# Kernel tuning notes

Hardware: AMD Instinct MI355X
Metric: run time of the kernel (lower is better)

## Reference

```python
import jax, jax.numpy as jnp
import numpy as np

EPS = 1e-6
ROPE_BASE = 10000.0

def setup_inputs() -> dict:
    key = jax.random.key(0)
    ks = jax.random.split(key, 6)
    B, S, D = 4, 4096, 1024
    NS, DS = 4, D // 4          # num_subspaces, subspace_dim
    H = 2 * DS                  # hidden_dim = ff_multiplier * subspace_dim
    scale = 0.02
    return {
        "x": jax.random.normal(ks[0], (B, S, D), dtype=jnp.float32),
        "norm_w": jnp.ones((D,), dtype=jnp.float32),
        # grouped SwiGLU weights: [NS, in, out] layout so we can einsum directly
        "Wg": jax.random.normal(ks[1], (NS, DS, H), dtype=jnp.float32) * scale,
        "Wu": jax.random.normal(ks[2], (NS, DS, H), dtype=jnp.float32) * scale,
        "Wd": jax.random.normal(ks[3], (NS, H, DS), dtype=jnp.float32) * scale,
        "Wo": jax.random.normal(ks[4], (D, D), dtype=jnp.float32) * scale,
    }

def _rope_cos_sin(S, D, dtype):
    inv_freq = 1.0 / (ROPE_BASE ** (jnp.arange(0, D, 2, dtype=jnp.float32) / D))
    freqs = jnp.arange(S, dtype=jnp.float32)[:, None] * inv_freq[None, :]  # [S, D/2]
    emb = jnp.concatenate([freqs, freqs], axis=-1)                          # [S, D]
    return jnp.cos(emb).astype(dtype), jnp.sin(emb).astype(dtype)

def reference(x, norm_w, Wg, Wu, Wd, Wo):
    B, S, D = x.shape
    NS, DS, H = Wg.shape
    # RMSNorm
    h = x * jax.lax.rsqrt(jnp.mean(x * x, axis=-1, keepdims=True) + EPS) * norm_w
    # RoPE over full hidden dim (rotate_half convention)
    cos, sin = _rope_cos_sin(S, D, x.dtype)
    half = D // 2
    rot = jnp.concatenate([-h[..., half:], h[..., :half]], axis=-1)
    h = h * cos[None] + rot * sin[None]
    # Grouped SwiGLU over NS independent subspaces
    hc = h.reshape(B, S, NS, DS)
    gate = jax.nn.silu(jnp.einsum('bsnd,ndh->bsnh', hc, Wg))
    up = jnp.einsum('bsnd,ndh->bsnh', hc, Wu)
    down = jnp.einsum('bsnh,nhd->bsnd', gate * up, Wd)
    out = down.reshape(B, S, D)
    # Final projection + residual
    return jnp.einsum('bsd,de->bse', out, Wo) + x
```

## Files before the change

### kernel.cpp

```cpp
#include <hip/hip_runtime.h>

typedef unsigned short u16;
typedef unsigned int   u32;

typedef float  f32x4  __attribute__((ext_vector_type(4)));
typedef __bf16 bf16x8 __attribute__((ext_vector_type(8)));

#define S_LEN  4096
#define DMODEL 1024
#define NSUB   4
#define DSUB   256
#define HFF    512
#define NTOK   16384

static_assert(sizeof(bf16x8) == 16, "frag size");

__device__ __forceinline__ u16 f2bf(float f) {
    union { float f; u32 u; } v; v.f = f;
    u32 r = (v.u + 0x7fffu + ((v.u >> 16) & 1u)) >> 16;
    return (u16)r;
}

#define MFMA16(a, b, c) __builtin_amdgcn_mfma_f32_16x16x32_bf16((a), (b), (c), 0, 0, 0)

__device__ __forceinline__ void gl_lds16(const void* g, void* l) {
    __builtin_amdgcn_global_load_lds(
        (const __attribute__((address_space(1))) void*)g,
        (__attribute__((address_space(3))) void*)l,
        16, 0, 0);
}
#define LGKM0 asm volatile("s_waitcnt lgkmcnt(0)" ::: "memory")
#define SCHED0 __builtin_amdgcn_sched_barrier(0)
#define SBAR __builtin_amdgcn_s_barrier()

__global__ __launch_bounds__(256) void k_prep(const float* __restrict__ Wg,
                                              const float* __restrict__ Wu,
                                              const float* __restrict__ Wd,
                                              const float* __restrict__ Wo,
                                              const float* __restrict__ x,
                                              const float* __restrict__ nw,
                                              u16* __restrict__ wgP,
                                              u16* __restrict__ wuP,
                                              u16* __restrict__ wdP,
                                              u16* __restrict__ woP,
                                              u16* __restrict__ h) {
    int bid = blockIdx.x;
    int tid = threadIdx.x;
    if (bid < 1280) {
        __shared__ float tl[32][65];
        const float* src; u16* dst; int K, C, rel;
        if (bid < 256)      { src = Wg; dst = wgP; K = 256;  C = 512;  rel = bid; }
        else if (bid < 512) { src = Wu; dst = wuP; K = 256;  C = 512;  rel = bid - 256; }
        else if (bid < 768) { src = Wd; dst = wdP; K = 512;  C = 256;  rel = bid - 512; }
        else                { src = Wo; dst = woP; K = 1024; C = 1024; rel = bid - 768; }
        int ncb = C >> 6, nkt = K >> 5;
        int cb = rel % ncb; int r2 = rel / ncb;
        int kt = r2 % nkt;  int b  = r2 / nkt;
        {
            int r = tid >> 3, c0 = (tid & 7) * 8;
            const float* s = src + ((size_t)(b * K + kt * 32 + r)) * C + cb * 64 + c0;
            float4 v0 = *(const float4*)(s);
            float4 v1 = *(const float4*)(s + 4);
            tl[r][c0 + 0] = v0.x; tl[r][c0 + 1] = v0.y; tl[r][c0 + 2] = v0.z; tl[r][c0 + 3] = v0.w;
            tl[r][c0 + 4] = v1.x; tl[r][c0 + 5] = v1.y; tl[r][c0 + 6] = v1.z; tl[r][c0 + 7] = v1.w;
        }
        __syncthreads();
        {
            int f = tid >> 6, l = tid & 63;
            union { u16 v[8]; uint4 q; } u;
#pragma unroll
            for (int j = 0; j < 8; ++j)
                u.v[j] = f2bf(tl[(l >> 4) * 8 + j][f * 16 + (l & 15)]);
            size_t ctile = (size_t)(b * (C >> 4) + cb * 4 + f);
            *(uint4*)(dst + (ctile * nkt + kt) * 512 + l * 8) = u.q;
        }
        return;
    }
    int tok = bid - 1280;
    int s = tok & (S_LEN - 1);
    int t = tid;
    const float* xr = x + (size_t)tok * DMODEL;
    float x0 = xr[t], x1 = xr[t + 256], x2 = xr[t + 512], x3 = xr[t + 768];
    float ss = x0 * x0 + x1 * x1 + x2 * x2 + x3 * x3;
#pragma unroll
    for (int o = 32; o > 0; o >>= 1) ss += __shfl_down(ss, o, 64);
    __shared__ float red[4];
    if ((t & 63) == 0) red[t >> 6] = ss;
    __syncthreads();
    float tot = red[0] + red[1] + red[2] + red[3];
    float sc = rsqrtf(tot * (1.0f / DMODEL) + 1e-6f);
    float n0 = x0 * sc * nw[t];
    float n1 = x1 * sc * nw[t + 256];
    float n2 = x2 * sc * nw[t + 512];
    float n3 = x3 * sc * nw[t + 768];
    const float C = -0.017988946039015984f;
    float sf = (float)s;
    float ang0 = sf * expf(C * (float)t);
    float ang1 = sf * expf(C * (float)(t + 256));
    float sn0, cs0, sn1, cs1;
    sincosf(ang0, &sn0, &cs0);
    sincosf(ang1, &sn1, &cs1);
    u16* hr = h + (size_t)tok * DMODEL;
    hr[t]       = f2bf(n0 * cs0 - n2 * sn0);
    hr[t + 256] = f2bf(n1 * cs1 - n3 * sn1);
    hr[t + 512] = f2bf(n2 * cs0 + n0 * sn0);
    hr[t + 768] = f2bf(n3 * cs1 + n1 * sn1);
}

__global__ __launch_bounds__(512, 2)
void k_swiglu(const u16* __restrict__ h,
              const u16* __restrict__ wgP,
              const u16* __restrict__ wuP,
              const u16* __restrict__ wdP,
              u16* __restrict__ dmid) {
    int bid = blockIdx.x;
    int mb = bid & 255, n = bid >> 8;
    int m0 = mb * 64;
    int tid = threadIdx.x;
    int lane = tid & 63, wid = tid >> 6;

    __shared__ u16 hA[64 * 256];
    __shared__ u16 sT[64 * 128];
    __shared__ u16 sW[8 * 2 * 1024];

    const u16* wg = wgP + (size_t)n * (32 * 8 * 512);
    const u16* wu = wuP + (size_t)n * (32 * 8 * 512);
    const u16* wd = wdP + (size_t)n * (16 * 16 * 512);
    u16* myW = sW + wid * 2048;

#define ISSUE(t)                                                               \
    do {                                                                       \
        if ((t) < 48) {                                                        \
            const int hcs = (t) / 12, rs = (t) % 12;                           \
            u16* db = myW + ((t) % 2) * 1024;                                  \
            if (rs < 8) {                                                      \
                size_t ct0 = (size_t)(hcs * 8 + wid);                          \
                gl_lds16(wg + (ct0 * 8 + rs) * 512 + lane * 8, db);            \
                gl_lds16(wu + (ct0 * 8 + rs) * 512 + lane * 8, db + 512);      \
            } else {                                                           \
                const int k2s = rs - 8;                                        \
                gl_lds16(wd + ((size_t)(wid * 2 + 0) * 16 + hcs * 4 + k2s) * 512 + lane * 8, db);        \
                gl_lds16(wd + ((size_t)(wid * 2 + 1) * 16 + hcs * 4 + k2s) * 512 + lane * 8, db + 512);  \
            }                                                                  \
        }                                                                      \
    } while (0)
#define VMW(t)                                                                 \
    do {                                                                       \
        if ((t) <= 46) asm volatile("s_waitcnt vmcnt(2)" ::: "memory");        \
        else           asm volatile("s_waitcnt vmcnt(0)" ::: "memory");        \
    } while (0)

    const u16* hbase = h + (size_t)m0 * DMODEL + n * DSUB;
    uint4 hv[4];
#pragma unroll
    for (int it = 0; it < 4; ++it) {
        int e = (tid + it * 512) * 8;
        int r = e >> 8, c = e & 255;
        hv[it] = *(const uint4*)(hbase + (size_t)r * DMODEL + c);
    }
    ISSUE(0); ISSUE(1);
#pragma unroll
    for (int it = 0; it < 4; ++it) {
        int e = (tid + it * 512) * 8;
        int r = e >> 8, c = e & 255;
        u32 off = ((u32)(r * 512 + c * 2)) ^ ((u32)(r & 7) << 4);
        *(uint4*)((char*)hA + off) = hv[it];
    }
    LGKM0; SBAR;

    const f32x4 zero = {0.f, 0.f, 0.f, 0.f};
    f32x4 accd[4][2];
#pragma unroll
    for (int a = 0; a < 4; ++a) { accd[a][0] = zero; accd[a][1] = zero; }

#pragma unroll
    for (int hc = 0; hc < 4; ++hc) {
        f32x4 accg[4], accu[4];
#pragma unroll
        for (int a = 0; a < 4; ++a) { accg[a] = zero; accu[a] = zero; }

#pragma unroll
        for (int ks = 0; ks < 8; ++ks) {
            const int t = hc * 12 + ks;
            VMW(t); SCHED0;
            const u16* rb = myW + (t % 2) * 1024;
            bf16x8 bg = *(const bf16x8*)(rb + lane * 8);
            bf16x8 bu = *(const bf16x8*)(rb + 512 + lane * 8);
            LGKM0; SCHED0;
            ISSUE(t + 2);
#pragma unroll
            for (int rt = 0; rt < 4; ++rt) {
                int arow = rt * 16 + (lane & 15);
                int k0 = ks * 32 + (lane >> 4) * 8;
                u32 off = ((u32)(arow * 512 + k0 * 2)) ^ ((u32)(arow & 7) << 4);
                bf16x8 afr = *(const bf16x8*)((const char*)hA + off);
                accg[rt] = MFMA16(afr, bg, accg[rt]);
                accu[rt] = MFMA16(afr, bu, accu[rt]);
            }
        }

#pragma unroll
        for (int rt = 0; rt < 4; ++rt) {
            int rbase = rt * 16 + (lane >> 4) * 4;
            int col = wid * 16 + (lane & 15);
#pragma unroll
            for (int q = 0; q < 4; ++q) {
                float g = accg[rt][q], u = accu[rt][q];
                float tv = (g / (1.0f + __expf(-g))) * u;
                int row = rbase + q;
                u32 off = ((u32)(row * 256 + col * 2)) ^ ((u32)(row & 7) << 4);
                *(u16*)((char*)sT + off) = f2bf(tv);
            }
        }
        LGKM0; SBAR;

#pragma unroll
        for (int k2 = 0; k2 < 4; ++k2) {
            const int t = hc * 12 + 8 + k2;
            VMW(t); SCHED0;
            const u16* rb = myW + (t % 2) * 1024;
            bf16x8 bd0 = *(const bf16x8*)(rb + lane * 8);
            bf16x8 bd1 = *(const bf16x8*)(rb + 512 + lane * 8);
            LGKM0; SCHED0;
            ISSUE(t + 2);
#pragma unroll
            for (int rt = 0; rt < 4; ++rt) {
                int arow = rt * 16 + (lane & 15);
                int k0 = k2 * 32 + (lane >> 4) * 8;
                u32 off = ((u32)(arow * 256 + k0 * 2)) ^ ((u32)(arow & 7) << 4);
                bf16x8 afr = *(const bf16x8*)((const char*)sT + off);
                accd[rt][0] = MFMA16(afr, bd0, accd[rt][0]);
                accd[rt][1] = MFMA16(afr, bd1, accd[rt][1]);
            }
        }
        LGKM0; SBAR;
    }
#undef ISSUE
#undef VMW

#pragma unroll
    for (int rt = 0; rt < 4; ++rt)
#pragma unroll
        for (int ct = 0; ct < 2; ++ct) {
            int rbase = m0 + rt * 16 + (lane >> 4) * 4;
            int col = n * DSUB + wid * 32 + ct * 16 + (lane & 15);
#pragma unroll
            for (int q = 0; q < 4; ++q)
                dmid[(size_t)(rbase + q) * DMODEL + col] = f2bf(accd[rt][ct][q]);
        }
}

__global__ __launch_bounds__(512, 2) void k_final(const u16* __restrict__ dmid,
                                                  const u16* __restrict__ woP,
                                                  const float* __restrict__ x,
                                                  float* __restrict__ out) {
    int bid = blockIdx.x;
    int mb = bid & 127, nb = bid >> 7;
    int m0 = mb * 128, n0 = nb * 256;
    int tid = threadIdx.x;
    int lane = tid & 63, wid = tid >> 6;
    int wr = wid >> 2, wc = wid & 3;

    __shared__ u16 sA[2][128 * 256];

    f32x4 acc[4][4];
    const u16* dbase = dmid + (size_t)m0 * DMODEL;

    uint4 stA[8], stB[8];
#pragma unroll
    for (int it = 0; it < 8; ++it) {
        int e = (tid + it * 512) * 8;
        int r = e >> 8, c = e & 255;
        stA[it] = *(const uint4*)(dbase + (size_t)r * DMODEL + c);
    }
#pragma unroll
    for (int rt = 0; rt < 4; ++rt)
#pragma unroll
        for (int ct = 0; ct < 4; ++ct) {
            int rbase = m0 + wr * 64 + rt * 16 + (lane >> 4) * 4;
            int col = n0 + wc * 64 + ct * 16 + (lane & 15);
#pragma unroll
            for (int q = 0; q < 4; ++q)
                acc[rt][ct][q] = x[(size_t)(rbase + q) * DMODEL + col];
        }
#pragma unroll
    for (int it = 0; it < 8; ++it) {
        int e = (tid + it * 512) * 8;
        int r = e >> 8, c = e & 255;
        u32 off = ((u32)(r * 512 + c * 2)) ^ ((u32)(r & 7) << 4);
        *(uint4*)((char*)sA[0] + off) = stA[it];
    }
#pragma unroll
    for (int it = 0; it < 8; ++it) {
        int e = (tid + it * 512) * 8;
        int r = e >> 8, c = e & 255;
        stB[it] = *(const uint4*)(dbase + (size_t)r * DMODEL + 256 + c);
    }

#pragma unroll
    for (int kc = 0; kc < 4; ++kc) {
        __syncthreads();
        if (kc < 3) {
#pragma unroll
            for (int it = 0; it < 8; ++it) {
                int e = (tid + it * 512) * 8;
                int r = e >> 8, c = e & 255;
                u32 off = ((u32)(r * 512 + c * 2)) ^ ((u32)(r & 7) << 4);
                uint4 v = (kc & 1) ? stA[it] : stB[it];
                *(uint4*)((char*)sA[(kc + 1) & 1] + off) = v;
            }
        }
        if (kc < 2) {
#pragma unroll
            for (int it = 0; it < 8; ++it) {
                int e = (tid + it * 512) * 8;
                int r = e >> 8, c = e & 255;
                uint4 v = *(const uint4*)(dbase + (size_t)r * DMODEL + (kc + 2) * 256 + c);
                if ((kc & 1) == 0) stA[it] = v; else stB[it] = v;
            }
        }

        const u16* sAc = (const u16*)sA[kc & 1];
        bf16x8 wf[2][4];
#pragma unroll
        for (int ct = 0; ct < 4; ++ct) {
            size_t ctile = (size_t)(nb * 16 + wc * 4 + ct);
            size_t ktile = (size_t)(kc * 8 + 0);
            wf[0][ct] = *(const bf16x8*)(woP + (ctile * 32 + ktile) * 512 + lane * 8);
        }
#pragma unroll
        for (int ks = 0; ks < 8; ++ks) {
            if (ks < 7) {
#pragma unroll
                for (int ct = 0; ct < 4; ++ct) {
                    size_t ctile = (size_t)(nb * 16 + wc * 4 + ct);
                    size_t ktile = (size_t)(kc * 8 + ks + 1);
                    wf[(ks + 1) & 1][ct] = *(const bf16x8*)(woP + (ctile * 32 + ktile) * 512 + lane * 8);
                }
            }
            bf16x8 afr[4];
#pragma unroll
            for (int rt = 0; rt < 4; ++rt) {
                int arow = wr * 64 + rt * 16 + (lane & 15);
                int k0 = ks * 32 + (lane >> 4) * 8;
                u32 off = ((u32)(arow * 512 + k0 * 2)) ^ ((u32)(arow & 7) << 4);
                afr[rt] = *(const bf16x8*)((const char*)sAc + off);
            }
#pragma unroll
            for (int ct = 0; ct < 4; ++ct)
#pragma unroll
                for (int rt = 0; rt < 4; ++rt)
                    acc[rt][ct] = MFMA16(afr[rt], wf[ks & 1][ct], acc[rt][ct]);
        }
    }

#pragma unroll
    for (int rt = 0; rt < 4; ++rt)
#pragma unroll
        for (int ct = 0; ct < 4; ++ct) {
            int rbase = m0 + wr * 64 + rt * 16 + (lane >> 4) * 4;
            int col = n0 + wc * 64 + ct * 16 + (lane & 15);
#pragma unroll
            for (int q = 0; q < 4; ++q) {
                size_t o = (size_t)(rbase + q) * DMODEL + col;
                out[o] = acc[rt][ct][q];
            }
        }
}

extern "C" void kernel_launch(void* const* d_in, const int* in_sizes, int n_in,
                              void* d_out, int out_size, void* d_ws, size_t ws_size,
                              hipStream_t stream) {
    const float* x  = (const float*)d_in[0];
    const float* nw = (const float*)d_in[1];
    const float* Wg = (const float*)d_in[2];
    const float* Wu = (const float*)d_in[3];
    const float* Wd = (const float*)d_in[4];
    const float* Wo = (const float*)d_in[5];
    float* out = (float*)d_out;

    char* ws = (char*)d_ws;
    const size_t MB = 1u << 20;
    u16* h    = (u16*)(ws);
    u16* wgP  = (u16*)(ws + 32 * MB);
    u16* wuP  = (u16*)(ws + 33 * MB);
    u16* wdP  = (u16*)(ws + 34 * MB);
    u16* woP  = (u16*)(ws + 35 * MB);
    u16* dmid = (u16*)(ws + 37 * MB);

    k_prep<<<1280 + NTOK, 256, 0, stream>>>(Wg, Wu, Wd, Wo, x, nw,
                                            wgP, wuP, wdP, woP, h);
    k_swiglu<<<256 * NSUB, 512, 0, stream>>>(h, wgP, wuP, wdP, dmid);
    k_final<<<128 * 4, 512, 0, stream>>>(dmid, woP, x, out);
}
```

Before: 168.6 us.

## Triple-buffer SwiGLU weight stream with double-width k-steps per stage

Reworks the per-wave weight prefetch in the grouped SwiGLU kernel. Each stage now loads two k-slices instead of one, and three buffers are kept in flight instead of two. This halves the number of waitcnt/LDS-read synchronisation points and deepens prefetch to hide global latency. In exchange the weight LDS footprint triples to 96KB per block, and launch bounds drop to one block per CU, which lowers occupancy.

```diff
diff --git a/kernel.cpp b/kernel.cpp
--- a/kernel.cpp
+++ b/kernel.cpp
@@ -107,7 +107,7 @@
     hr[t + 768] = f2bf(n3 * cs1 + n1 * sn1);
 }
 
-__global__ __launch_bounds__(512, 2)
+__global__ __launch_bounds__(512, 1)
 void k_swiglu(const u16* __restrict__ h,
               const u16* __restrict__ wgP,
               const u16* __restrict__ wuP,
@@ -121,33 +121,39 @@
 
     __shared__ u16 hA[64 * 256];
     __shared__ u16 sT[64 * 128];
-    __shared__ u16 sW[8 * 2 * 1024];
+    __shared__ u16 sW[8 * 3 * 2048];
 
     const u16* wg = wgP + (size_t)n * (32 * 8 * 512);
     const u16* wu = wuP + (size_t)n * (32 * 8 * 512);
     const u16* wd = wdP + (size_t)n * (16 * 16 * 512);
-    u16* myW = sW + wid * 2048;
+    u16* myW = sW + wid * 6144;
 
 #define ISSUE(t)                                                               \
     do {                                                                       \
-        if ((t) < 48) {                                                        \
-            const int hcs = (t) / 12, rs = (t) % 12;                           \
-            u16* db = myW + ((t) % 2) * 1024;                                  \
-            if (rs < 8) {                                                      \
+        if ((t) < 24) {                                                        \
+            const int hcs = (t) / 6, rs = (t) % 6;                             \
+            u16* db = myW + ((t) % 3) * 2048;                                  \
+            if (rs < 4) {                                                      \
                 size_t ct0 = (size_t)(hcs * 8 + wid);                          \
-                gl_lds16(wg + (ct0 * 8 + rs) * 512 + lane * 8, db);            \
-                gl_lds16(wu + (ct0 * 8 + rs) * 512 + lane * 8, db + 512);      \
+                const int ks0 = rs * 2;                                        \
+                gl_lds16(wg + (ct0 * 8 + ks0) * 512 + lane * 8, db);           \
+                gl_lds16(wu + (ct0 * 8 + ks0) * 512 + lane * 8, db + 512);     \
+                gl_lds16(wg + (ct0 * 8 + ks0 + 1) * 512 + lane * 8, db + 1024);\
+                gl_lds16(wu + (ct0 * 8 + ks0 + 1) * 512 + lane * 8, db + 1536);\
             } else {                                                           \
-                const int k2s = rs - 8;                                        \
-                gl_lds16(wd + ((size_t)(wid * 2 + 0) * 16 + hcs * 4 + k2s) * 512 + lane * 8, db);        \
-                gl_lds16(wd + ((size_t)(wid * 2 + 1) * 16 + hcs * 4 + k2s) * 512 + lane * 8, db + 512);  \
+                const int k20 = (rs - 4) * 2;                                  \
+                gl_lds16(wd + ((size_t)(wid * 2 + 0) * 16 + hcs * 4 + k20) * 512 + lane * 8, db);            \
+                gl_lds16(wd + ((size_t)(wid * 2 + 1) * 16 + hcs * 4 + k20) * 512 + lane * 8, db + 512);      \
+                gl_lds16(wd + ((size_t)(wid * 2 + 0) * 16 + hcs * 4 + k20 + 1) * 512 + lane * 8, db + 1024); \
+                gl_lds16(wd + ((size_t)(wid * 2 + 1) * 16 + hcs * 4 + k20 + 1) * 512 + lane * 8, db + 1536); \
             }                                                                  \
         }                                                                      \
     } while (0)
 #define VMW(t)                                                                 \
     do {                                                                       \
-        if ((t) <= 46) asm volatile("s_waitcnt vmcnt(2)" ::: "memory");        \
-        else           asm volatile("s_waitcnt vmcnt(0)" ::: "memory");        \
+        if ((t) <= 21)      asm volatile("s_waitcnt vmcnt(8)" ::: "memory");   \
+        else if ((t) == 22) asm volatile("s_waitcnt vmcnt(4)" ::: "memory");   \
+        else                asm volatile("s_waitcnt vmcnt(0)" ::: "memory");   \
     } while (0)
 
     const u16* hbase = h + (size_t)m0 * DMODEL + n * DSUB;
@@ -158,7 +164,7 @@
         int r = e >> 8, c = e & 255;
         hv[it] = *(const uint4*)(hbase + (size_t)r * DMODEL + c);
     }
-    ISSUE(0); ISSUE(1);
+    ISSUE(0); ISSUE(1); ISSUE(2);
 #pragma unroll
     for (int it = 0; it < 4; ++it) {
         int e = (tid + it * 512) * 8;
@@ -180,22 +186,28 @@
         for (int a = 0; a < 4; ++a) { accg[a] = zero; accu[a] = zero; }
 
 #pragma unroll
-        for (int ks = 0; ks < 8; ++ks) {
-            const int t = hc * 12 + ks;
+        for (int ks2 = 0; ks2 < 4; ++ks2) {
+            const int t = hc * 6 + ks2;
             VMW(t); SCHED0;
-            const u16* rb = myW + (t % 2) * 1024;
-            bf16x8 bg = *(const bf16x8*)(rb + lane * 8);
-            bf16x8 bu = *(const bf16x8*)(rb + 512 + lane * 8);
+            const u16* rb = myW + (t % 3) * 2048;
+            bf16x8 bg0 = *(const bf16x8*)(rb + lane * 8);
+            bf16x8 bu0 = *(const bf16x8*)(rb + 512 + lane * 8);
+            bf16x8 bg1 = *(const bf16x8*)(rb + 1024 + lane * 8);
+            bf16x8 bu1 = *(const bf16x8*)(rb + 1536 + lane * 8);
             LGKM0; SCHED0;
-            ISSUE(t + 2);
-#pragma unroll
-            for (int rt = 0; rt < 4; ++rt) {
-                int arow = rt * 16 + (lane & 15);
-                int k0 = ks * 32 + (lane >> 4) * 8;
-                u32 off = ((u32)(arow * 512 + k0 * 2)) ^ ((u32)(arow & 7) << 4);
-                bf16x8 afr = *(const bf16x8*)((const char*)hA + off);
-                accg[rt] = MFMA16(afr, bg, accg[rt]);
-                accu[rt] = MFMA16(afr, bu, accu[rt]);
+            ISSUE(t + 3);
+#pragma unroll
+            for (int half = 0; half < 2; ++half) {
+                const int ks = ks2 * 2 + half;
+#pragma unroll
+                for (int rt = 0; rt < 4; ++rt) {
+                    int arow = rt * 16 + (lane & 15);
+                    int k0 = ks * 32 + (lane >> 4) * 8;
+                    u32 off = ((u32)(arow * 512 + k0 * 2)) ^ ((u32)(arow & 7) << 4);
+                    bf16x8 afr = *(const bf16x8*)((const char*)hA + off);
+                    accg[rt] = MFMA16(afr, half ? bg1 : bg0, accg[rt]);
+                    accu[rt] = MFMA16(afr, half ? bu1 : bu0, accu[rt]);
+                }
             }
         }
 
@@ -215,22 +227,28 @@
         LGKM0; SBAR;
 
 #pragma unroll
-        for (int k2 = 0; k2 < 4; ++k2) {
-            const int t = hc * 12 + 8 + k2;
+        for (int k22 = 0; k22 < 2; ++k22) {
+            const int t = hc * 6 + 4 + k22;
             VMW(t); SCHED0;
-            const u16* rb = myW + (t % 2) * 1024;
-            bf16x8 bd0 = *(const bf16x8*)(rb + lane * 8);
-            bf16x8 bd1 = *(const bf16x8*)(rb + 512 + lane * 8);
+            const u16* rb = myW + (t % 3) * 2048;
+            bf16x8 bdA0 = *(const bf16x8*)(rb + lane * 8);
+            bf16x8 bdB0 = *(const bf16x8*)(rb + 512 + lane * 8);
+            bf16x8 bdA1 = *(const bf16x8*)(rb + 1024 + lane * 8);
+            bf16x8 bdB1 = *(const bf16x8*)(rb + 1536 + lane * 8);
             LGKM0; SCHED0;
-            ISSUE(t + 2);
-#pragma unroll
-            for (int rt = 0; rt < 4; ++rt) {
-                int arow = rt * 16 + (lane & 15);
-                int k0 = k2 * 32 + (lane >> 4) * 8;
-                u32 off = ((u32)(arow * 256 + k0 * 2)) ^ ((u32)(arow & 7) << 4);
-                bf16x8 afr = *(const bf16x8*)((const char*)sT + off);
-                accd[rt][0] = MFMA16(afr, bd0, accd[rt][0]);
-                accd[rt][1] = MFMA16(afr, bd1, accd[rt][1]);
+            ISSUE(t + 3);
+#pragma unroll
+            for (int half = 0; half < 2; ++half) {
+                const int k2 = k22 * 2 + half;
+#pragma unroll
+                for (int rt = 0; rt < 4; ++rt) {
+                    int arow = rt * 16 + (lane & 15);
+                    int k0 = k2 * 32 + (lane >> 4) * 8;
+                    u32 off = ((u32)(arow * 256 + k0 * 2)) ^ ((u32)(arow & 7) << 4);
+                    bf16x8 afr = *(const bf16x8*)((const char*)sT + off);
+                    accd[rt][0] = MFMA16(afr, half ? bdA1 : bdA0, accd[rt][0]);
+                    accd[rt][1] = MFMA16(afr, half ? bdB1 : bdB0, accd[rt][1]);
+                }
             }
         }
         LGKM0; SBAR;
```

Result: faster. 158.4 us (-6.1%).
